# Optimization experiments

Measured on AMD Instinct MI355X. Metric: run time of the kernel, lower is better.

The kernel has to match this reference:

```python
import jax, jax.numpy as jnp
import numpy as np

N = 300000   # total points
B = 8        # scenes per batch
INC = 64     # channels
HID = INC // 4  # MLP hidden (reduction=4)
S = 64       # voxel grid extent per axis


def _build_neighbor_table(batch_idx, coords):
    """Kernel map for a 3x3x3 stride-1 sparse conv: for each point, index of the
    point at each of the 27 integer offsets (N = missing -> zero pad row)."""
    base = S + 2
    keys = (((batch_idx.astype(np.int64) * base + coords[:, 0]) * base
             + coords[:, 1]) * base + coords[:, 2])
    order = np.argsort(keys)
    skeys = keys[order]
    offs = np.array([(dx, dy, dz) for dx in (-1, 0, 1)
                     for dy in (-1, 0, 1) for dz in (-1, 0, 1)], dtype=np.int64)
    off_keys = (offs[:, 0] * base + offs[:, 1]) * base + offs[:, 2]  # [27]
    q = keys[:, None] + off_keys[None, :]                             # [N,27]
    pos = np.searchsorted(skeys, q)
    posc = np.minimum(pos, N - 1)
    valid = (pos < N) & (skeys[posc] == q)
    nbr = np.where(valid, order[posc], N).astype(np.int32)
    return nbr


def setup_inputs() -> dict:
    rng = np.random.default_rng(0)
    batch_idx = np.sort(rng.integers(0, B, size=N)).astype(np.int32)
    coords = rng.integers(1, S - 1, size=(N, 3))
    nbr_idx = _build_neighbor_table(batch_idx, coords)
    key = jax.random.key(0)
    k = jax.random.split(key, 6)
    return {
        "F": jax.random.normal(k[0], (N, INC), dtype=jnp.float32),
        "batch_idx": jnp.asarray(batch_idx),
        "nbr_idx": jnp.asarray(nbr_idx),
        "W1": jax.random.normal(k[1], (INC, HID), dtype=jnp.float32) * 0.05,
        "b1": jax.random.normal(k[2], (HID,), dtype=jnp.float32) * 0.05,
        "W2": jax.random.normal(k[3], (HID, INC), dtype=jnp.float32) * 0.05,
        "b2": jax.random.normal(k[4], (INC,), dtype=jnp.float32) * 0.05,
        "conv_w": jax.random.normal(k[5], (27, 2, 1), dtype=jnp.float32) * 0.1,
    }


def reference(F, batch_idx, nbr_idx, W1, b1, W2, b2, conv_w):
    # ---- channel attention: per-batch segmented mean & max, broadcast back ----
    counts = jax.ops.segment_sum(jnp.ones((N,), F.dtype), batch_idx, num_segments=B)
    seg_mean = jax.ops.segment_sum(F, batch_idx, num_segments=B) / counts[:, None]
    seg_max = jax.ops.segment_max(F, batch_idx, num_segments=B)
    avg = seg_mean[batch_idx]   # [N, INC]
    mx = seg_max[batch_idx]     # [N, INC]

    def mlp(a):
        return jax.nn.relu(a @ W1 + b1) @ W2 + b2

    gate = jax.nn.sigmoid(mlp(avg) + mlp(mx))
    z = F * gate                # [N, INC]

    # ---- spatial attention: channel mean/max -> 2ch sparse 3^3 conv -> gate ----
    sm = jnp.stack([z.mean(axis=1), z.max(axis=1)], axis=1)   # [N, 2] (mean, max)
    smp = jnp.concatenate([sm, jnp.zeros((1, 2), sm.dtype)], axis=0)  # pad row N
    gathered = smp[nbr_idx]                                    # [N, 27, 2]
    c = jnp.einsum('nkc,kco->no', gathered, conv_w)            # [N, 1]
    return z * jax.nn.sigmoid(c)
```

## Files before the change

### kernel.cpp

```cpp
#include <hip/hip_runtime.h>
#include <math.h>

#define INC 64
#define HID 16
#define NB 8

__device__ __forceinline__ void atomicMaxF(float* addr, float val) {
    if (val >= 0.0f) atomicMax((int*)addr, __float_as_int(val));
    else             atomicMin((unsigned int*)addr, __float_as_uint(val));
}

__device__ __forceinline__ void acc4(float4& sum, float4& mx, const float4 v) {
    sum.x += v.x; sum.y += v.y; sum.z += v.z; sum.w += v.w;
    mx.x = fmaxf(mx.x, v.x); mx.y = fmaxf(mx.y, v.y);
    mx.z = fmaxf(mx.z, v.z); mx.w = fmaxf(mx.w, v.w);
}

__global__ void k_init(float* seg_sum, float* seg_max, int* counts, float* sm_pad) {
    int t = threadIdx.x;
    if (t < NB * INC) { seg_sum[t] = 0.0f; seg_max[t] = -INFINITY; }
    else if (t < NB * INC + NB) counts[t - NB * INC] = 0;
    else if (t < NB * INC + NB + 2) sm_pad[t - NB * INC - NB] = 0.0f;
}

__global__ void k_reduce(const float* __restrict__ F, const int* __restrict__ bidx,
                         float* __restrict__ seg_sum, float* __restrict__ seg_max,
                         int* __restrict__ counts, int N, int CHUNK) {
    int lane = threadIdx.x & 63;
    int wave = (blockIdx.x * blockDim.x + threadIdx.x) >> 6;
    int start = wave * CHUNK;
    if (start >= N) return;
    int pend = min(start + CHUNK, N);
    int sub = lane >> 4;
    int ch  = (lane & 15) << 2;

    int bfirst = bidx[start];
    int blast  = bidx[pend - 1];

    if (bfirst == blast) {
        float4 sum = make_float4(0.f, 0.f, 0.f, 0.f);
        float4 mx  = make_float4(-INFINITY, -INFINITY, -INFINITY, -INFINITY);
        const float* fb = F + (size_t)sub * INC + ch;
        int p = start;
        for (; p + 16 <= pend; p += 16) {
            const float* fp = fb + (size_t)p * INC;
            float4 v0 = *reinterpret_cast<const float4*>(fp);
            float4 v1 = *reinterpret_cast<const float4*>(fp + 4 * INC);
            float4 v2 = *reinterpret_cast<const float4*>(fp + 8 * INC);
            float4 v3 = *reinterpret_cast<const float4*>(fp + 12 * INC);
            acc4(sum, mx, v0); acc4(sum, mx, v1);
            acc4(sum, mx, v2); acc4(sum, mx, v3);
        }
        for (; p < pend; p += 4) {
            float4 v = *reinterpret_cast<const float4*>(fb + (size_t)p * INC);
            acc4(sum, mx, v);
        }
        #pragma unroll
        for (int msk = 16; msk < 64; msk <<= 1) {
            sum.x += __shfl_xor(sum.x, msk); sum.y += __shfl_xor(sum.y, msk);
            sum.z += __shfl_xor(sum.z, msk); sum.w += __shfl_xor(sum.w, msk);
            mx.x = fmaxf(mx.x, __shfl_xor(mx.x, msk));
            mx.y = fmaxf(mx.y, __shfl_xor(mx.y, msk));
            mx.z = fmaxf(mx.z, __shfl_xor(mx.z, msk));
            mx.w = fmaxf(mx.w, __shfl_xor(mx.w, msk));
        }
        if (sub == 0) {
            float* ss = seg_sum + bfirst * INC + ch;
            atomicAdd(ss + 0, sum.x); atomicAdd(ss + 1, sum.y);
            atomicAdd(ss + 2, sum.z); atomicAdd(ss + 3, sum.w);
            float* sx = seg_max + bfirst * INC + ch;
            atomicMaxF(sx + 0, mx.x); atomicMaxF(sx + 1, mx.y);
            atomicMaxF(sx + 2, mx.z); atomicMaxF(sx + 3, mx.w);
            if (lane == 0) atomicAdd(&counts[bfirst], pend - start);
        }
        return;
    }

    bool isCnt = (lane & 15) == 0;
    float4 sum = make_float4(0.f, 0.f, 0.f, 0.f);
    float4 mx  = make_float4(-INFINITY, -INFINITY, -INFINITY, -INFINITY);
    int cnt = 0, cur = -1;
    for (int p = start; p < pend; p += 4) {
        int pp = p + sub;
        int b = bidx[pp];
        if (b != cur) {
            if (cur >= 0) {
                float* ss = seg_sum + cur * INC + ch;
                atomicAdd(ss + 0, sum.x); atomicAdd(ss + 1, sum.y);
                atomicAdd(ss + 2, sum.z); atomicAdd(ss + 3, sum.w);
                float* sx = seg_max + cur * INC + ch;
                atomicMaxF(sx + 0, mx.x); atomicMaxF(sx + 1, mx.y);
                atomicMaxF(sx + 2, mx.z); atomicMaxF(sx + 3, mx.w);
                if (isCnt && cnt) atomicAdd(&counts[cur], cnt);
            }
            sum = make_float4(0.f, 0.f, 0.f, 0.f);
            mx  = make_float4(-INFINITY, -INFINITY, -INFINITY, -INFINITY);
            cnt = 0; cur = b;
        }
        const float4 v = *reinterpret_cast<const float4*>(F + (size_t)pp * INC + ch);
        acc4(sum, mx, v);
        cnt += (int)isCnt;
    }
    if (cur >= 0) {
        float* ss = seg_sum + cur * INC + ch;
        atomicAdd(ss + 0, sum.x); atomicAdd(ss + 1, sum.y);
        atomicAdd(ss + 2, sum.z); atomicAdd(ss + 3, sum.w);
        float* sx = seg_max + cur * INC + ch;
        atomicMaxF(sx + 0, mx.x); atomicMaxF(sx + 1, mx.y);
        atomicMaxF(sx + 2, mx.z); atomicMaxF(sx + 3, mx.w);
        if (isCnt && cnt) atomicAdd(&counts[cur], cnt);
    }
}

__global__ void k_gate(const float* __restrict__ seg_sum, const float* __restrict__ seg_max,
                       const int* __restrict__ counts,
                       const float* __restrict__ W1, const float* __restrict__ b1,
                       const float* __restrict__ W2, const float* __restrict__ b2,
                       float* __restrict__ gate) {
    __shared__ float s_avg[NB * INC], s_mx[NB * INC];
    __shared__ float s_W1[INC * HID], s_W2[HID * INC];
    __shared__ float s_ha[NB * HID], s_hm[NB * HID];
    int t = threadIdx.x;
    s_W1[t] = W1[t]; s_W1[t + 512] = W1[t + 512];
    s_W2[t] = W2[t]; s_W2[t + 512] = W2[t + 512];
    {
        int b = t >> 6;
        float c = (float)counts[b];
        s_avg[t] = seg_sum[t] / c;
        s_mx[t]  = seg_max[t];
    }
    __syncthreads();
    if (t < NB * HID) {
        int b = t >> 4, j = t & (HID - 1);
        float ha = b1[j], hm = b1[j];
        #pragma unroll
        for (int c = 0; c < INC; ++c) {
            float w = s_W1[c * HID + j];
            ha += s_avg[b * INC + c] * w;
            hm += s_mx[b * INC + c] * w;
        }
        s_ha[t] = fmaxf(ha, 0.f);
        s_hm[t] = fmaxf(hm, 0.f);
    }
    __syncthreads();
    {
        int b = t >> 6, c = t & 63;
        float o = 2.f * b2[c];
        #pragma unroll
        for (int j = 0; j < HID; ++j)
            o += (s_ha[b * HID + j] + s_hm[b * HID + j]) * W2[j * INC + c];
        gate[t] = 1.f / (1.f + expf(-o));
    }
}

__global__ void k_sm(const float* __restrict__ F, const int* __restrict__ bidx,
                     const float* __restrict__ gate, float* __restrict__ sm,
                     int N, int CHUNK) {
    int lane = threadIdx.x & 63;
    int wave = (blockIdx.x * blockDim.x + threadIdx.x) >> 6;
    int start = wave * CHUNK;
    if (start >= N) return;
    int pend = min(start + CHUNK, N);
    int sub = lane >> 4, ch = (lane & 15) << 2;
    bool wr = (lane & 15) == 0;

    int bfirst = bidx[start];
    int blast  = bidx[pend - 1];

    if (bfirst == blast) {
        const float4 g = *reinterpret_cast<const float4*>(gate + bfirst * INC + ch);
        const float* fb = F + (size_t)sub * INC + ch;
        int p = start;
        for (; p + 16 <= pend; p += 16) {
            const float* fp = fb + (size_t)p * INC;
            float4 v0 = *reinterpret_cast<const float4*>(fp);
            float4 v1 = *reinterpret_cast<const float4*>(fp + 4 * INC);
            float4 v2 = *reinterpret_cast<const float4*>(fp + 8 * INC);
            float4 v3 = *reinterpret_cast<const float4*>(fp + 12 * INC);
            float s0, s1, s2, s3, m0, m1, m2, m3;
            {
                float4 z = make_float4(v0.x*g.x, v0.y*g.y, v0.z*g.z, v0.w*g.w);
                s0 = z.x + z.y + z.z + z.w; m0 = fmaxf(fmaxf(z.x, z.y), fmaxf(z.z, z.w));
            }
            {
                float4 z = make_float4(v1.x*g.x, v1.y*g.y, v1.z*g.z, v1.w*g.w);
                s1 = z.x + z.y + z.z + z.w; m1 = fmaxf(fmaxf(z.x, z.y), fmaxf(z.z, z.w));
            }
            {
                float4 z = make_float4(v2.x*g.x, v2.y*g.y, v2.z*g.z, v2.w*g.w);
                s2 = z.x + z.y + z.z + z.w; m2 = fmaxf(fmaxf(z.x, z.y), fmaxf(z.z, z.w));
            }
            {
                float4 z = make_float4(v3.x*g.x, v3.y*g.y, v3.z*g.z, v3.w*g.w);
                s3 = z.x + z.y + z.z + z.w; m3 = fmaxf(fmaxf(z.x, z.y), fmaxf(z.z, z.w));
            }
            #pragma unroll
            for (int msk = 1; msk < 16; msk <<= 1) {
                s0 += __shfl_xor(s0, msk); m0 = fmaxf(m0, __shfl_xor(m0, msk));
                s1 += __shfl_xor(s1, msk); m1 = fmaxf(m1, __shfl_xor(m1, msk));
                s2 += __shfl_xor(s2, msk); m2 = fmaxf(m2, __shfl_xor(m2, msk));
                s3 += __shfl_xor(s3, msk); m3 = fmaxf(m3, __shfl_xor(m3, msk));
            }
            if (wr) {
                *reinterpret_cast<float2*>(sm + (size_t)(p + sub) * 2)      = make_float2(s0 * (1.f/64.f), m0);
                *reinterpret_cast<float2*>(sm + (size_t)(p + 4 + sub) * 2)  = make_float2(s1 * (1.f/64.f), m1);
                *reinterpret_cast<float2*>(sm + (size_t)(p + 8 + sub) * 2)  = make_float2(s2 * (1.f/64.f), m2);
                *reinterpret_cast<float2*>(sm + (size_t)(p + 12 + sub) * 2) = make_float2(s3 * (1.f/64.f), m3);
            }
        }
        for (; p < pend; p += 4) {
            float4 v = *reinterpret_cast<const float4*>(fb + (size_t)p * INC);
            float4 z = make_float4(v.x*g.x, v.y*g.y, v.z*g.z, v.w*g.w);
            float s = z.x + z.y + z.z + z.w;
            float m = fmaxf(fmaxf(z.x, z.y), fmaxf(z.z, z.w));
            #pragma unroll
            for (int msk = 1; msk < 16; msk <<= 1) {
                s += __shfl_xor(s, msk); m = fmaxf(m, __shfl_xor(m, msk));
            }
            if (wr) *reinterpret_cast<float2*>(sm + (size_t)(p + sub) * 2) = make_float2(s * (1.f/64.f), m);
        }
        return;
    }

    for (int p = start; p < pend; p += 4) {
        int pp = p + sub;
        int b = bidx[pp];
        float4 v = *reinterpret_cast<const float4*>(F + (size_t)pp * INC + ch);
        float4 g = *reinterpret_cast<const float4*>(gate + b * INC + ch);
        float4 z = make_float4(v.x*g.x, v.y*g.y, v.z*g.z, v.w*g.w);
        float s = z.x + z.y + z.z + z.w;
        float m = fmaxf(fmaxf(z.x, z.y), fmaxf(z.z, z.w));
        #pragma unroll
        for (int msk = 1; msk < 16; msk <<= 1) {
            s += __shfl_xor(s, msk); m = fmaxf(m, __shfl_xor(m, msk));
        }
        if (wr) *reinterpret_cast<float2*>(sm + (size_t)pp * 2) = make_float2(s * (1.f/64.f), m);
    }
}

__global__ void k_out(const float* __restrict__ F, const int* __restrict__ bidx,
                      const int* __restrict__ nbr, const float* __restrict__ gate,
                      const float* __restrict__ sm, const float* __restrict__ cw,
                      float* __restrict__ out, int N, int CHUNK) {
    int lane = threadIdx.x & 63;
    int j = lane & 15;
    int sub = lane >> 4, ch = (lane & 15) << 2;
    float2 cwa = make_float2(cw[2 * j], cw[2 * j + 1]);
    float2 cwb = (j < 11) ? make_float2(cw[2 * (16 + j)], cw[2 * (16 + j) + 1])
                          : make_float2(0.f, 0.f);
    int wave = (blockIdx.x * blockDim.x + threadIdx.x) >> 6;
    int start = wave * CHUNK;
    if (start >= N) return;
    int pend = min(start + CHUNK, N);

    int bfirst = bidx[start];
    int blast  = bidx[pend - 1];

    if (bfirst == blast) {
        const float4 g = *reinterpret_cast<const float4*>(gate + bfirst * INC + ch);
        int pp = start + sub;
        int i1 = nbr[pp * 27 + j];
        int i2 = (j < 11) ? nbr[pp * 27 + 16 + j] : N;
        for (int p = start; p < pend; p += 4) {
            float2 a = *reinterpret_cast<const float2*>(sm + (size_t)i1 * 2);
            float2 b = *reinterpret_cast<const float2*>(sm + (size_t)i2 * 2);
            int np = p + 4 + sub; if (np >= N) np = N - 1;
            int ni1 = nbr[np * 27 + j];
            int ni2 = (j < 11) ? nbr[np * 27 + 16 + j] : N;
            float4 v = *reinterpret_cast<const float4*>(F + (size_t)(p + sub) * INC + ch);
            float cpart = a.x * cwa.x + a.y * cwa.y + b.x * cwb.x + b.y * cwb.y;
            #pragma unroll
            for (int msk = 1; msk < 16; msk <<= 1) cpart += __shfl_xor(cpart, msk);
            float sig = 1.f / (1.f + expf(-cpart));
            float4 o = make_float4(v.x * g.x * sig, v.y * g.y * sig,
                                   v.z * g.z * sig, v.w * g.w * sig);
            *reinterpret_cast<float4*>(out + (size_t)(p + sub) * INC + ch) = o;
            i1 = ni1; i2 = ni2;
        }
        return;
    }

    for (int p = start; p < pend; p += 4) {
        int pp = p + sub;
        int rb = pp * 27;
        int i1 = nbr[rb + j];
        int i2 = (j < 11) ? nbr[rb + 16 + j] : N;
        float2 a = *reinterpret_cast<const float2*>(sm + (size_t)i1 * 2);
        float2 b = *reinterpret_cast<const float2*>(sm + (size_t)i2 * 2);
        float cpart = a.x * cwa.x + a.y * cwa.y + b.x * cwb.x + b.y * cwb.y;
        #pragma unroll
        for (int msk = 1; msk < 16; msk <<= 1) cpart += __shfl_xor(cpart, msk);
        float sig = 1.f / (1.f + expf(-cpart));
        int bb = bidx[pp];
        float4 v = *reinterpret_cast<const float4*>(F + (size_t)pp * INC + ch);
        float4 g = *reinterpret_cast<const float4*>(gate + bb * INC + ch);
        float4 o = make_float4(v.x * g.x * sig, v.y * g.y * sig,
                               v.z * g.z * sig, v.w * g.w * sig);
        *reinterpret_cast<float4*>(out + (size_t)pp * INC + ch) = o;
    }
}

extern "C" void kernel_launch(void* const* d_in, const int* in_sizes, int n_in,
                              void* d_out, int out_size, void* d_ws, size_t ws_size,
                              hipStream_t stream) {
    const float* F    = (const float*)d_in[0];
    const int*   bidx = (const int*)d_in[1];
    const int*   nbr  = (const int*)d_in[2];
    const float* W1   = (const float*)d_in[3];
    const float* b1   = (const float*)d_in[4];
    const float* W2   = (const float*)d_in[5];
    const float* b2   = (const float*)d_in[6];
    const float* cw   = (const float*)d_in[7];
    float* out = (float*)d_out;
    int N = in_sizes[1];

    float* ws      = (float*)d_ws;
    float* seg_sum = ws;
    float* seg_max = ws + NB * INC;
    int*   counts  = (int*)(ws + 2 * NB * INC);
    float* gate    = ws + 2 * NB * INC + 16;
    float* sm      = ws + 3 * NB * INC + 32;

    k_init<<<1, 1024, 0, stream>>>(seg_sum, seg_max, counts, sm + (size_t)N * 2);

    {
        const int waves = 4096;
        int chunk = ((N + waves * 16 - 1) / (waves * 16)) * 16;
        k_reduce<<<1024, 256, 0, stream>>>(F, bidx, seg_sum, seg_max, counts, N, chunk);
    }

    k_gate<<<1, 512, 0, stream>>>(seg_sum, seg_max, counts, W1, b1, W2, b2, gate);

    {
        const int waves = 8192;
        int chunk = ((N + waves * 16 - 1) / (waves * 16)) * 16;
        k_sm<<<2048, 256, 0, stream>>>(F, bidx, gate, sm, N, chunk);
        k_out<<<2048, 256, 0, stream>>>(F, bidx, nbr, gate, sm, cw, out, N, chunk);
    }
}
```

Before: 286.0 us.

## Block-level reduction in k_reduce and larger per-wave chunks across kernels

k_reduce now checks whether a whole 4-wave block lies in one batch segment. If so, it keeps four independent accumulators per lane, combines the waves through shared memory, and issues one set of atomics per block instead of one per wave. Launch sizes change: fewer waves with larger chunks for all three streaming kernels, plus sched_barrier hints and unroll-1 pragmas so the loads issue ahead of the arithmetic. k_gate reads W2 from shared memory, which assumes s_W2 exists in the unseen part of the kernel. Fewer waves may lower occupancy and latency hiding on the memory-bound passes.

Result: faster. 250.9 us (-12.3%).

```diff
diff --git a/kernel.cpp b/kernel.cpp
--- a/kernel.cpp
+++ b/kernel.cpp
@@ -26,32 +26,95 @@
 __global__ void k_reduce(const float* __restrict__ F, const int* __restrict__ bidx,
                          float* __restrict__ seg_sum, float* __restrict__ seg_max,
                          int* __restrict__ counts, int N, int CHUNK) {
+    __shared__ float4 lsum[4][16];
+    __shared__ float4 lmax[4][16];
+
     int lane = threadIdx.x & 63;
-    int wave = (blockIdx.x * blockDim.x + threadIdx.x) >> 6;
-    int start = wave * CHUNK;
-    if (start >= N) return;
-    int pend = min(start + CHUNK, N);
+    int wid  = threadIdx.x >> 6;
+    int blockStart = blockIdx.x * (CHUNK * 4);
+    if (blockStart >= N) return;
+    int blockEnd = min(blockStart + CHUNK * 4, N);
+    int start = blockStart + wid * CHUNK;
+    bool active = start < N;
+    int pend = active ? min(start + CHUNK, N) : start;
+
     int sub = lane >> 4;
     int ch  = (lane & 15) << 2;
 
+    int bblk = bidx[blockStart];
+    bool blockUniform = (bidx[blockEnd - 1] == bblk);
+
+    if (blockUniform) {
+        float4 s0 = make_float4(0.f,0.f,0.f,0.f), s1 = s0, s2 = s0, s3 = s0;
+        float4 m0 = make_float4(-INFINITY,-INFINITY,-INFINITY,-INFINITY);
+        float4 m1 = m0, m2 = m0, m3 = m0;
+        if (active) {
+            const float* fb = F + (size_t)sub * INC + ch;
+            int p = start;
+            #pragma unroll 1
+            for (; p + 16 <= pend; p += 16) {
+                const float* fp = fb + (size_t)p * INC;
+                float4 v0 = *reinterpret_cast<const float4*>(fp);
+                float4 v1 = *reinterpret_cast<const float4*>(fp + 4 * INC);
+                float4 v2 = *reinterpret_cast<const float4*>(fp + 8 * INC);
+                float4 v3 = *reinterpret_cast<const float4*>(fp + 12 * INC);
+                __builtin_amdgcn_sched_barrier(0);
+                acc4(s0, m0, v0); acc4(s1, m1, v1);
+                acc4(s2, m2, v2); acc4(s3, m3, v3);
+            }
+            #pragma unroll 1
+            for (; p < pend; p += 4) {
+                float4 v = *reinterpret_cast<const float4*>(fb + (size_t)p * INC);
+                acc4(s0, m0, v);
+            }
+        }
+        s0.x += s1.x + s2.x + s3.x; s0.y += s1.y + s2.y + s3.y;
+        s0.z += s1.z + s2.z + s3.z; s0.w += s1.w + s2.w + s3.w;
+        m0.x = fmaxf(fmaxf(m0.x, m1.x), fmaxf(m2.x, m3.x));
+        m0.y = fmaxf(fmaxf(m0.y, m1.y), fmaxf(m2.y, m3.y));
+        m0.z = fmaxf(fmaxf(m0.z, m1.z), fmaxf(m2.z, m3.z));
+        m0.w = fmaxf(fmaxf(m0.w, m1.w), fmaxf(m2.w, m3.w));
+        #pragma unroll
+        for (int msk = 16; msk < 64; msk <<= 1) {
+            s0.x += __shfl_xor(s0.x, msk); s0.y += __shfl_xor(s0.y, msk);
+            s0.z += __shfl_xor(s0.z, msk); s0.w += __shfl_xor(s0.w, msk);
+            m0.x = fmaxf(m0.x, __shfl_xor(m0.x, msk));
+            m0.y = fmaxf(m0.y, __shfl_xor(m0.y, msk));
+            m0.z = fmaxf(m0.z, __shfl_xor(m0.z, msk));
+            m0.w = fmaxf(m0.w, __shfl_xor(m0.w, msk));
+        }
+        if (lane < 16) { lsum[wid][lane] = s0; lmax[wid][lane] = m0; }
+        __syncthreads();
+        if (wid == 0 && lane < 16) {
+            float4 a0 = lsum[0][lane], a1 = lsum[1][lane], a2 = lsum[2][lane], a3 = lsum[3][lane];
+            float4 x0 = lmax[0][lane], x1 = lmax[1][lane], x2 = lmax[2][lane], x3 = lmax[3][lane];
+            float4 S = make_float4(a0.x+a1.x+a2.x+a3.x, a0.y+a1.y+a2.y+a3.y,
+                                   a0.z+a1.z+a2.z+a3.z, a0.w+a1.w+a2.w+a3.w);
+            float4 M = make_float4(fmaxf(fmaxf(x0.x,x1.x),fmaxf(x2.x,x3.x)),
+                                   fmaxf(fmaxf(x0.y,x1.y),fmaxf(x2.y,x3.y)),
+                                   fmaxf(fmaxf(x0.z,x1.z),fmaxf(x2.z,x3.z)),
+                                   fmaxf(fmaxf(x0.w,x1.w),fmaxf(x2.w,x3.w)));
+            float* ss = seg_sum + bblk * INC + (lane << 2);
+            atomicAdd(ss + 0, S.x); atomicAdd(ss + 1, S.y);
+            atomicAdd(ss + 2, S.z); atomicAdd(ss + 3, S.w);
+            float* sx = seg_max + bblk * INC + (lane << 2);
+            atomicMaxF(sx + 0, M.x); atomicMaxF(sx + 1, M.y);
+            atomicMaxF(sx + 2, M.z); atomicMaxF(sx + 3, M.w);
+            if (lane == 0) atomicAdd(&counts[bblk], blockEnd - blockStart);
+        }
+        return;
+    }
+
+    if (!active) return;
     int bfirst = bidx[start];
     int blast  = bidx[pend - 1];
 
     if (bfirst == blast) {
-        float4 sum = make_float4(0.f, 0.f, 0.f, 0.f);
-        float4 mx  = make_float4(-INFINITY, -INFINITY, -INFINITY, -INFINITY);
+        float4 sum = make_float4(0.f,0.f,0.f,0.f);
+        float4 mx  = make_float4(-INFINITY,-INFINITY,-INFINITY,-INFINITY);
         const float* fb = F + (size_t)sub * INC + ch;
-        int p = start;
-        for (; p + 16 <= pend; p += 16) {
-            const float* fp = fb + (size_t)p * INC;
-            float4 v0 = *reinterpret_cast<const float4*>(fp);
-            float4 v1 = *reinterpret_cast<const float4*>(fp + 4 * INC);
-            float4 v2 = *reinterpret_cast<const float4*>(fp + 8 * INC);
-            float4 v3 = *reinterpret_cast<const float4*>(fp + 12 * INC);
-            acc4(sum, mx, v0); acc4(sum, mx, v1);
-            acc4(sum, mx, v2); acc4(sum, mx, v3);
-        }
-        for (; p < pend; p += 4) {
+        #pragma unroll 1
+        for (int p = start; p < pend; p += 4) {
             float4 v = *reinterpret_cast<const float4*>(fb + (size_t)p * INC);
             acc4(sum, mx, v);
         }
@@ -77,8 +140,8 @@
     }
 
     bool isCnt = (lane & 15) == 0;
-    float4 sum = make_float4(0.f, 0.f, 0.f, 0.f);
-    float4 mx  = make_float4(-INFINITY, -INFINITY, -INFINITY, -INFINITY);
+    float4 sum = make_float4(0.f,0.f,0.f,0.f);
+    float4 mx  = make_float4(-INFINITY,-INFINITY,-INFINITY,-INFINITY);
     int cnt = 0, cur = -1;
     for (int p = start; p < pend; p += 4) {
         int pp = p + sub;
@@ -93,8 +156,8 @@
                 atomicMaxF(sx + 2, mx.z); atomicMaxF(sx + 3, mx.w);
                 if (isCnt && cnt) atomicAdd(&counts[cur], cnt);
             }
-            sum = make_float4(0.f, 0.f, 0.f, 0.f);
-            mx  = make_float4(-INFINITY, -INFINITY, -INFINITY, -INFINITY);
+            sum = make_float4(0.f,0.f,0.f,0.f);
+            mx  = make_float4(-INFINITY,-INFINITY,-INFINITY,-INFINITY);
             cnt = 0; cur = b;
         }
         const float4 v = *reinterpret_cast<const float4*>(F + (size_t)pp * INC + ch);
@@ -148,7 +211,7 @@
         float o = 2.f * b2[c];
         #pragma unroll
         for (int j = 0; j < HID; ++j)
-            o += (s_ha[b * HID + j] + s_hm[b * HID + j]) * W2[j * INC + c];
+            o += (s_ha[b * HID + j] + s_hm[b * HID + j]) * s_W2[j * INC + c];
         gate[t] = 1.f / (1.f + expf(-o));
     }
 }
@@ -171,12 +234,14 @@
         const float4 g = *reinterpret_cast<const float4*>(gate + bfirst * INC + ch);
         const float* fb = F + (size_t)sub * INC + ch;
         int p = start;
+        #pragma unroll 1
         for (; p + 16 <= pend; p += 16) {
             const float* fp = fb + (size_t)p * INC;
             float4 v0 = *reinterpret_cast<const float4*>(fp);
             float4 v1 = *reinterpret_cast<const float4*>(fp + 4 * INC);
             float4 v2 = *reinterpret_cast<const float4*>(fp + 8 * INC);
             float4 v3 = *reinterpret_cast<const float4*>(fp + 12 * INC);
+            __builtin_amdgcn_sched_barrier(0);
             float s0, s1, s2, s3, m0, m1, m2, m3;
             {
                 float4 z = make_float4(v0.x*g.x, v0.y*g.y, v0.z*g.z, v0.w*g.w);
@@ -208,6 +273,7 @@
                 *reinterpret_cast<float2*>(sm + (size_t)(p + 12 + sub) * 2) = make_float2(s3 * (1.f/64.f), m3);
             }
         }
+        #pragma unroll 1
         for (; p < pend; p += 4) {
             float4 v = *reinterpret_cast<const float4*>(fb + (size_t)p * INC);
             float4 z = make_float4(v.x*g.x, v.y*g.y, v.z*g.z, v.w*g.w);
@@ -261,6 +327,7 @@
         int pp = start + sub;
         int i1 = nbr[pp * 27 + j];
         int i2 = (j < 11) ? nbr[pp * 27 + 16 + j] : N;
+        #pragma unroll 1
         for (int p = start; p < pend; p += 4) {
             float2 a = *reinterpret_cast<const float2*>(sm + (size_t)i1 * 2);
             float2 b = *reinterpret_cast<const float2*>(sm + (size_t)i2 * 2);
@@ -268,6 +335,7 @@
             int ni1 = nbr[np * 27 + j];
             int ni2 = (j < 11) ? nbr[np * 27 + 16 + j] : N;
             float4 v = *reinterpret_cast<const float4*>(F + (size_t)(p + sub) * INC + ch);
+            __builtin_amdgcn_sched_barrier(0);
             float cpart = a.x * cwa.x + a.y * cwa.y + b.x * cwb.x + b.y * cwb.y;
             #pragma unroll
             for (int msk = 1; msk < 16; msk <<= 1) cpart += __shfl_xor(cpart, msk);
@@ -324,17 +392,19 @@
     k_init<<<1, 1024, 0, stream>>>(seg_sum, seg_max, counts, sm + (size_t)N * 2);
 
     {
+        const int waves = 2048;
+        int chunk = ((N + waves * 16 - 1) / (waves * 16)) * 16;
+        int blocks = (N + chunk * 4 - 1) / (chunk * 4);
+        k_reduce<<<blocks, 256, 0, stream>>>(F, bidx, seg_sum, seg_max, counts, N, chunk);
+    }
+
+    k_gate<<<1, 512, 0, stream>>>(seg_sum, seg_max, counts, W1, b1, W2, b2, gate);
+
+    {
         const int waves = 4096;
         int chunk = ((N + waves * 16 - 1) / (waves * 16)) * 16;
-        k_reduce<<<1024, 256, 0, stream>>>(F, bidx, seg_sum, seg_max, counts, N, chunk);
-    }
-
-    k_gate<<<1, 512, 0, stream>>>(seg_sum, seg_max, counts, W1, b1, W2, b2, gate);
-
-    {
-        const int waves = 8192;
-        int chunk = ((N + waves * 16 - 1) / (waves * 16)) * 16;
-        k_sm<<<2048, 256, 0, stream>>>(F, bidx, gate, sm, N, chunk);
-        k_out<<<2048, 256, 0, stream>>>(F, bidx, nbr, gate, sm, cw, out, N, chunk);
-    }
-}
+        int blocks = (N + chunk * 4 - 1) / (chunk * 4);
+        k_sm<<<blocks, 256, 0, stream>>>(F, bidx, gate, sm, N, chunk);
+        k_out<<<blocks, 256, 0, stream>>>(F, bidx, nbr, gate, sm, cw, out, N, chunk);
+    }
+}
```
